# Performance work log

Measured on AMD Instinct MI355X. Metric: run time of the kernel, lower is better.

The kernel has to match this reference:

```python
import jax, jax.numpy as jnp
import numpy as np
from jax.scipy.special import logsumexp

S, D, K, R, P = 500, 768, 16, 256, 64  # seq_len, bert_dim, out_dim, n_pairs, max wordpieces/entity


def setup_inputs() -> dict:
    key = jax.random.key(0)
    k1, k2, k3, k4, k5, k6 = jax.random.split(key, 6)
    word_embeddings = jax.random.normal(k1, (S, D), jnp.float32)
    # kaiming_normal_ fan_in = D*K (last two dims collapsed); gain sqrt(2) for relu
    W = jax.random.normal(k2, (D, K, D), jnp.float32) * np.float32((2.0 / (K * D)) ** 0.5)
    idx1 = jax.random.randint(k3, (R, P), 0, S)
    idx2 = jax.random.randint(k4, (R, P), 0, S)
    # ragged mention lengths -> padding masks (at least 1 valid wordpiece)
    len1 = jax.random.randint(k5, (R,), 1, P + 1)
    len2 = jax.random.randint(k6, (R,), 1, P + 1)
    pos = jnp.arange(P)
    mask1 = (pos[None, :] < len1[:, None]).astype(jnp.float32)
    mask2 = (pos[None, :] < len2[:, None]).astype(jnp.float32)
    return {"word_embeddings": word_embeddings, "W": W, "idx1": idx1, "idx2": idx2,
            "mask1": mask1, "mask2": mask2}


def reference(word_embeddings, W, idx1, idx2, mask1, mask2):
    # gather ragged mention wordpieces (padded to P per entity)
    e1 = word_embeddings[idx1]  # [R, P, D]
    e2 = word_embeddings[idx2]  # [R, P, D]
    # biaffine: z[r,k,p,q] = e1[r,p,:] @ W[:,k,:] @ e2[r,q,:]
    zh = jnp.einsum('rpd,dke->rpke', e1, W)      # [R, P, K, D]
    z = jnp.einsum('rpke,rqe->rkpq', zh, e2)     # [R, K, P, P]
    # logsumexp pooling over all valid (p, q) mention-token pairs
    b = mask1[:, None, :, None] * mask2[:, None, None, :]  # [R, 1, P, P]
    scores = logsumexp(z, axis=(2, 3), b=b)      # [R, K]
    return scores
```

## Files before the change

### kernel.cpp

```cpp
#include <hip/hip_runtime.h>
#include <math.h>

#define S_ 500
#define D_ 768
#define K_ 16
#define R_ 256
#define P_ 64
#define NT 12

typedef unsigned short ushort_t;
typedef __attribute__((ext_vector_type(8))) short short8;
typedef __attribute__((ext_vector_type(4))) float floatx4;

__device__ inline ushort_t f2bf(float x) {
  unsigned int u = __float_as_uint(x);
  u += 0x7fffu + ((u >> 16) & 1u);
  return (ushort_t)(u >> 16);
}

#define GLD_LDS16(g, l)                                                        \
  __builtin_amdgcn_global_load_lds(                                            \
      (const __attribute__((address_space(1))) void*)(g),                      \
      (__attribute__((address_space(3))) void*)(l), 16, 0, 0)

#define ASM_BARRIER asm volatile("s_barrier" ::: "memory")
#define WAIT_VM8 asm volatile("s_waitcnt vmcnt(8)" ::: "memory")
#define WAIT_VM6 asm volatile("s_waitcnt vmcnt(6)" ::: "memory")
#define WAIT_VM0 asm volatile("s_waitcnt vmcnt(0)" ::: "memory")

__global__ __launch_bounds__(256) void prep(const float* __restrict__ WE,
                                            const float* __restrict__ W,
                                            ushort_t* __restrict__ WEb,
                                            ushort_t* __restrict__ Wt) {
  const int t = threadIdx.x;
  if (blockIdx.x < 384) {
    int gid = blockIdx.x * 256 + t;
    int row = gid / 192;
    ushort4 o = {0, 0, 0, 0};
    if (row < S_) {
      float4 v = *(const float4*)(WE + (size_t)gid * 4);
      o.x = f2bf(v.x); o.y = f2bf(v.y); o.z = f2bf(v.z); o.w = f2bf(v.w);
    }
    *(ushort4*)(WEb + (size_t)gid * 4) = o;
    return;
  }
  __shared__ float tile[64][68];
  const int tb = blockIdx.x - 384;
  const int n0 = (tb % 192) * 64, d0 = (tb / 192) * 64;
  {
    const int r = t >> 2, cbase = (t & 3) * 16;
#pragma unroll
    for (int i = 0; i < 4; i++) {
      float4 v = *(const float4*)(W + (size_t)(d0 + r) * 12288 + n0 + cbase + i * 4);
      *(float4*)&tile[r][cbase + i * 4] = v;
    }
  }
  __syncthreads();
  {
    const int bc = t & 15;
    const int br4 = (t >> 4) * 4;
    float4 tv[4];
#pragma unroll
    for (int ii = 0; ii < 4; ii++)
      tv[ii] = *(const float4*)&tile[bc * 4 + ii][br4];
#pragma unroll
    for (int j = 0; j < 4; j++) {
      ushort4 o;
      o.x = f2bf(((const float*)&tv[0])[j]);
      o.y = f2bf(((const float*)&tv[1])[j]);
      o.z = f2bf(((const float*)&tv[2])[j]);
      o.w = f2bf(((const float*)&tv[3])[j]);
      *(ushort4*)(Wt + (size_t)(n0 + br4 + j) * 768 + d0 + bc * 4) = o;
    }
  }
}

__global__ __launch_bounds__(256, 2) void mm0_bt(const ushort_t* __restrict__ A,
                                                 const ushort_t* __restrict__ Bm,
                                                 ushort_t* __restrict__ C) {
  __shared__ ushort_t As[2][2][128 * 32];
  __shared__ ushort_t Bs[2][2][128 * 32];
  const int tid = threadIdx.x;
  const int wave = tid >> 6, lane = tid & 63;
  const int m0 = blockIdx.y * 128, n0 = blockIdx.x * 128;
  const int wm = (wave & 1) * 64, wn = (wave >> 1) * 64;
  const int col = lane & 15, quad = lane >> 4;

  floatx4 acc[4][4];
#pragma unroll
  for (int i = 0; i < 4; i++)
#pragma unroll
    for (int j = 0; j < 4; j++)
#pragma unroll
      for (int e = 0; e < 4; e++) acc[i][j][e] = 0.f;

  const int srow = wave * 32 + (lane >> 2);
  const int scol = (lane & 3) * 8;
  const ushort_t* ga0 = A + (size_t)(m0 + srow) * D_ + scol;
  const ushort_t* gb0 = Bm + (size_t)(n0 + srow) * D_ + scol;
  const int ldsbase = (wave * 32) * 32;

#define ISSUE_TILE0(t_, buf_)                                                  \
  do {                                                                         \
    const ushort_t* ga = ga0 + (t_)*64;                                        \
    const ushort_t* gb = gb0 + (t_)*64;                                        \
    GLD_LDS16(ga, &As[buf_][0][ldsbase]);                                      \
    GLD_LDS16(ga + 16 * D_, &As[buf_][0][ldsbase + 16 * 32]);                  \
    GLD_LDS16(ga + 32, &As[buf_][1][ldsbase]);                                 \
    GLD_LDS16(ga + 32 + 16 * D_, &As[buf_][1][ldsbase + 16 * 32]);             \
    GLD_LDS16(gb, &Bs[buf_][0][ldsbase]);                                      \
    GLD_LDS16(gb + 16 * D_, &Bs[buf_][0][ldsbase + 16 * 32]);                  \
    GLD_LDS16(gb + 32, &Bs[buf_][1][ldsbase]);                                 \
    GLD_LDS16(gb + 32 + 16 * D_, &Bs[buf_][1][ldsbase + 16 * 32]);             \
  } while (0)

  ISSUE_TILE0(0, 0);
  for (int t = 0; t < NT; ++t) {
    const int cur = t & 1;
    if (t + 1 < NT) {
      ISSUE_TILE0(t + 1, cur ^ 1);
      WAIT_VM8;
    } else {
      WAIT_VM0;
    }
    ASM_BARRIER;
#pragma unroll
    for (int s = 0; s < 2; ++s) {
      short8 a[4], b[4];
#pragma unroll
      for (int i = 0; i < 4; i++)
        a[i] = *(const short8*)&As[cur][s][(wm + i * 16 + col) * 32 + quad * 8];
#pragma unroll
      for (int j = 0; j < 4; j++)
        b[j] = *(const short8*)&Bs[cur][s][(wn + j * 16 + col) * 32 + quad * 8];
#pragma unroll
      for (int i = 0; i < 4; i++)
#pragma unroll
        for (int j = 0; j < 4; j++)
          acc[i][j] = __builtin_amdgcn_mfma_f32_16x16x32_bf16(b[j], a[i], acc[i][j], 0, 0, 0);
    }
    ASM_BARRIER;
  }
#undef ISSUE_TILE0

#pragma unroll
  for (int i = 0; i < 4; i++) {
    int m = m0 + wm + i * 16 + col;
#pragma unroll
    for (int j = 0; j < 4; j++) {
      int n = n0 + wn + j * 16 + quad * 4;
      ushort4 o;
      o.x = f2bf(acc[i][j][0]); o.y = f2bf(acc[i][j][1]);
      o.z = f2bf(acc[i][j][2]); o.w = f2bf(acc[i][j][3]);
      *(ushort4*)(C + (size_t)m * 12288 + n) = o;
    }
  }
}

__global__ __launch_bounds__(256, 2) void mm1_bt(const ushort_t* __restrict__ A,
                                                 const ushort_t* __restrict__ Bm,
                                                 ushort_t* __restrict__ G) {
  __shared__ ushort_t As[2][2][128 * 32];
  __shared__ ushort_t Bs[2][2][64 * 32];
  const int tid = threadIdx.x;
  const int wave = tid >> 6, lane = tid & 63;
  const int lin = blockIdx.x + (blockIdx.y << 3);
  const int yb = ((lin & 7) << 3) | (lin >> 6);
  const int xb = (lin >> 3) & 7;
  const int m0 = yb * 128, n0 = xb * 64;
  const int wm = (wave & 1) * 64, wn = (wave >> 1) * 32;
  const int col = lane & 15, quad = lane >> 4;

  floatx4 acc[4][2];
#pragma unroll
  for (int i = 0; i < 4; i++)
#pragma unroll
    for (int j = 0; j < 2; j++)
#pragma unroll
      for (int e = 0; e < 4; e++) acc[i][j][e] = 0.f;

  const int lrow = lane >> 2, scol = (lane & 3) * 8;
  const ushort_t* ga0 = A + (size_t)(m0 + wave * 32 + lrow) * D_ + scol;
  const ushort_t* gb0 = Bm + (size_t)(n0 + wave * 16 + lrow) * D_ + scol;
  const int aoff = (wave * 32) * 32;
  const int boff = (wave * 16) * 32;

#define ISSUE_TILE1(t_, buf_)                                                  \
  do {                                                                         \
    _Pragma("unroll") for (int s_ = 0; s_ < 2; s_++) {                         \
      const ushort_t* ga = ga0 + (t_)*64 + s_ * 32;                            \
      const ushort_t* gb = gb0 + (t_)*64 + s_ * 32;                            \
      GLD_LDS16(ga, &As[buf_][s_][aoff]);                                      \
      GLD_LDS16(ga + 16 * D_, &As[buf_][s_][aoff + 16 * 32]);                  \
      GLD_LDS16(gb, &Bs[buf_][s_][boff]);                                      \
    }                                                                          \
  } while (0)

  ISSUE_TILE1(0, 0);
  for (int t = 0; t < NT; ++t) {
    const int cur = t & 1;
    if (t + 1 < NT) {
      ISSUE_TILE1(t + 1, cur ^ 1);
      WAIT_VM6;
    } else {
      WAIT_VM0;
    }
    ASM_BARRIER;
#pragma unroll
    for (int s = 0; s < 2; ++s) {
      short8 a[4], b[2];
#pragma unroll
      for (int i = 0; i < 4; i++)
        a[i] = *(const short8*)&As[cur][s][(wm + i * 16 + col) * 32 + quad * 8];
#pragma unroll
      for (int j = 0; j < 2; j++)
        b[j] = *(const short8*)&Bs[cur][s][(wn + j * 16 + col) * 32 + quad * 8];
#pragma unroll
      for (int i = 0; i < 4; i++)
#pragma unroll
        for (int j = 0; j < 2; j++)
          acc[i][j] = __builtin_amdgcn_mfma_f32_16x16x32_bf16(a[i], b[j], acc[i][j], 0, 0, 0);
    }
    ASM_BARRIER;
  }
#undef ISSUE_TILE1

#pragma unroll
  for (int i = 0; i < 4; i++) {
    int s1 = (m0 + wm + i * 16) >> 4;
#pragma unroll
    for (int j = 0; j < 2; j++) {
      int s2 = n0 + wn + j * 16 + col;
      if (s1 < S_ && s2 < S_) {
        ushort4 o;
        o.x = f2bf(acc[i][j][0]); o.y = f2bf(acc[i][j][1]);
        o.z = f2bf(acc[i][j][2]); o.w = f2bf(acc[i][j][3]);
        *(ushort4*)(G + (((size_t)s1 * S_ + s2) << 4) + quad * 4) = o;
      }
    }
  }
}

__global__ __launch_bounds__(512) void lse_kernel(const ushort_t* __restrict__ G,
                                                  const int* __restrict__ idx1,
                                                  const int* __restrict__ idx2,
                                                  const float* __restrict__ mask1,
                                                  const float* __restrict__ mask2,
                                                  float* __restrict__ out) {
  const int r = blockIdx.x;
  const int tid = threadIdx.x;
  __shared__ int b1[P_], b2[P_];
  __shared__ int s_len1, s_len2;
  __shared__ float wmx[8][K_], wsum[8][K_];

  if (tid < 64) {
    float mv = mask1[r * P_ + tid];
    unsigned long long bal = __ballot(mv > 0.5f);
    if (tid == 0) s_len1 = (int)__popcll(bal);
    b1[tid] = idx1[r * P_ + tid] * (S_ * K_);
  } else if (tid < 128) {
    int q = tid - 64;
    float mv = mask2[r * P_ + q];
    unsigned long long bal = __ballot(mv > 0.5f);
    if (q == 0) s_len2 = (int)__popcll(bal);
    b2[q] = idx2[r * P_ + q] * K_;
  }
  __syncthreads();
  const int len2 = s_len2;
  const int total = s_len1 * len2;

  float m[K_], s[K_];
#pragma unroll
  for (int k = 0; k < K_; k++) { m[k] = -3.0e38f; s[k] = 0.f; }

  for (int i = tid; i < total; i += 512) {
    int p = i / len2;
    int q = i - p * len2;
    const uint4* g4 = (const uint4*)(G + b1[p] + b2[q]);
    uint4 w0 = g4[0], w1 = g4[1];
    unsigned int uu[8] = {w0.x, w0.y, w0.z, w0.w, w1.x, w1.y, w1.z, w1.w};
    float z[K_];
#pragma unroll
    for (int h = 0; h < 8; h++) {
      z[2 * h + 0] = __uint_as_float(uu[h] << 16);
      z[2 * h + 1] = __uint_as_float(uu[h] & 0xffff0000u);
    }
#pragma unroll
    for (int k = 0; k < K_; k++) {
      float d = z[k] - m[k];
      float e = __expf(-fabsf(d));
      bool up = d > 0.f;
      s[k] = up ? __fmaf_rn(s[k], e, 1.f) : (s[k] + e);
      m[k] = up ? z[k] : m[k];
    }
  }

#pragma unroll
  for (int off = 1; off < 64; off <<= 1) {
#pragma unroll
    for (int k = 0; k < K_; k++) {
      float mo = __shfl_xor(m[k], off, 64);
      float so = __shfl_xor(s[k], off, 64);
      float d = mo - m[k];
      float e = __expf(-fabsf(d));
      bool up = d > 0.f;
      s[k] = up ? __fmaf_rn(s[k], e, so) : __fmaf_rn(so, e, s[k]);
      m[k] = up ? mo : m[k];
    }
  }
  const int wave = tid >> 6, lane = tid & 63;
  if (lane == 0) {
#pragma unroll
    for (int k = 0; k < K_; k++) { wmx[wave][k] = m[k]; wsum[wave][k] = s[k]; }
  }
  __syncthreads();
  if (tid < K_) {
    float M = -3.0e38f, Ssum = 0.f;
#pragma unroll
    for (int w = 0; w < 8; w++) {
      float mo = wmx[w][tid], so = wsum[w][tid];
      float d = mo - M;
      float e = __expf(-fabsf(d));
      bool up = d > 0.f;
      Ssum = up ? __fmaf_rn(Ssum, e, so) : __fmaf_rn(so, e, Ssum);
      M = up ? mo : M;
    }
    out[r * K_ + tid] = M + __logf(Ssum);
  }
}

extern "C" void kernel_launch(void* const* d_in, const int* in_sizes, int n_in,
                              void* d_out, int out_size, void* d_ws, size_t ws_size,
                              hipStream_t stream) {
  const float* WE    = (const float*)d_in[0];
  const float* W     = (const float*)d_in[1];
  const int*   idx1  = (const int*)d_in[2];
  const int*   idx2  = (const int*)d_in[3];
  const float* mask1 = (const float*)d_in[4];
  const float* mask2 = (const float*)d_in[5];
  float* out = (float*)d_out;

  ushort_t* WEb   = (ushort_t*)d_ws;
  ushort_t* Wt    = WEb + (size_t)512 * 768;
  ushort_t* projb = Wt + (size_t)12288 * 768;
  ushort_t* G     = projb + (size_t)8192 * 768;

  prep<<<384 + 2304, 256, 0, stream>>>(WE, W, WEb, Wt);
  mm0_bt<<<dim3(96, 4), 256, 0, stream>>>(WEb, Wt, projb);
  mm1_bt<<<dim3(8, 64), 256, 0, stream>>>(projb, WEb, G);
  lse_kernel<<<R_, 512, 0, stream>>>(G, idx1, idx2, mask1, mask2, out);
}
```

Measured before the change: 134.0 us.

## Fuse W transpose and bf16 conversion into first GEMM's B-tile loads

Drops the separate prep pass that transposed W into a bf16 Wt buffer. The first GEMM now reads fp32 W directly into registers, converts pairs with v_cvt_pk_bf16_f32, and writes them into an XOR-swizzled LDS layout, prefetching the next tile's registers while computing the current one. This removes a full read and write of the 37MB W tensor through a temporary, at the cost of register-staged B loads, a __syncthreads per k-step, and fp32-width global reads inside the GEMM.

```diff
diff --git a/kernel.cpp b/kernel.cpp
--- a/kernel.cpp
+++ b/kernel.cpp
@@ -11,6 +11,7 @@
 typedef unsigned short ushort_t;
 typedef __attribute__((ext_vector_type(8))) short short8;
 typedef __attribute__((ext_vector_type(4))) float floatx4;
+typedef __attribute__((ext_vector_type(4))) float fx4;
 
 __device__ inline ushort_t f2bf(float x) {
   unsigned int u = __float_as_uint(x);
@@ -18,66 +19,37 @@
   return (ushort_t)(u >> 16);
 }
 
+__device__ inline unsigned int cvtpk(float lo, float hi) {
+  unsigned int r;
+  asm("v_cvt_pk_bf16_f32 %0, %1, %2" : "=v"(r) : "v"(lo), "v"(hi));
+  return r;
+}
+
 #define GLD_LDS16(g, l)                                                        \
   __builtin_amdgcn_global_load_lds(                                            \
       (const __attribute__((address_space(1))) void*)(g),                      \
       (__attribute__((address_space(3))) void*)(l), 16, 0, 0)
 
 #define ASM_BARRIER asm volatile("s_barrier" ::: "memory")
-#define WAIT_VM8 asm volatile("s_waitcnt vmcnt(8)" ::: "memory")
 #define WAIT_VM6 asm volatile("s_waitcnt vmcnt(6)" ::: "memory")
 #define WAIT_VM0 asm volatile("s_waitcnt vmcnt(0)" ::: "memory")
 
 __global__ __launch_bounds__(256) void prep(const float* __restrict__ WE,
-                                            const float* __restrict__ W,
-                                            ushort_t* __restrict__ WEb,
-                                            ushort_t* __restrict__ Wt) {
+                                            ushort_t* __restrict__ WEb) {
   const int t = threadIdx.x;
-  if (blockIdx.x < 384) {
-    int gid = blockIdx.x * 256 + t;
-    int row = gid / 192;
-    ushort4 o = {0, 0, 0, 0};
-    if (row < S_) {
-      float4 v = *(const float4*)(WE + (size_t)gid * 4);
-      o.x = f2bf(v.x); o.y = f2bf(v.y); o.z = f2bf(v.z); o.w = f2bf(v.w);
-    }
-    *(ushort4*)(WEb + (size_t)gid * 4) = o;
-    return;
-  }
-  __shared__ float tile[64][68];
-  const int tb = blockIdx.x - 384;
-  const int n0 = (tb % 192) * 64, d0 = (tb / 192) * 64;
-  {
-    const int r = t >> 2, cbase = (t & 3) * 16;
-#pragma unroll
-    for (int i = 0; i < 4; i++) {
-      float4 v = *(const float4*)(W + (size_t)(d0 + r) * 12288 + n0 + cbase + i * 4);
-      *(float4*)&tile[r][cbase + i * 4] = v;
-    }
-  }
-  __syncthreads();
-  {
-    const int bc = t & 15;
-    const int br4 = (t >> 4) * 4;
-    float4 tv[4];
-#pragma unroll
-    for (int ii = 0; ii < 4; ii++)
-      tv[ii] = *(const float4*)&tile[bc * 4 + ii][br4];
-#pragma unroll
-    for (int j = 0; j < 4; j++) {
-      ushort4 o;
-      o.x = f2bf(((const float*)&tv[0])[j]);
-      o.y = f2bf(((const float*)&tv[1])[j]);
-      o.z = f2bf(((const float*)&tv[2])[j]);
-      o.w = f2bf(((const float*)&tv[3])[j]);
-      *(ushort4*)(Wt + (size_t)(n0 + br4 + j) * 768 + d0 + bc * 4) = o;
-    }
-  }
-}
-
-__global__ __launch_bounds__(256, 2) void mm0_bt(const ushort_t* __restrict__ A,
-                                                 const ushort_t* __restrict__ Bm,
-                                                 ushort_t* __restrict__ C) {
+  int gid = blockIdx.x * 256 + t;
+  int row = gid / 192;
+  ushort4 o = {0, 0, 0, 0};
+  if (row < S_) {
+    float4 v = *(const float4*)(WE + (size_t)gid * 4);
+    o.x = f2bf(v.x); o.y = f2bf(v.y); o.z = f2bf(v.z); o.w = f2bf(v.w);
+  }
+  *(ushort4*)(WEb + (size_t)gid * 4) = o;
+}
+
+__global__ __launch_bounds__(256, 2) void mm0_fused(const ushort_t* __restrict__ A,
+                                                    const float* __restrict__ Wf,
+                                                    ushort_t* __restrict__ C) {
   __shared__ ushort_t As[2][2][128 * 32];
   __shared__ ushort_t Bs[2][2][128 * 32];
   const int tid = threadIdx.x;
@@ -97,33 +69,54 @@
   const int srow = wave * 32 + (lane >> 2);
   const int scol = (lane & 3) * 8;
   const ushort_t* ga0 = A + (size_t)(m0 + srow) * D_ + scol;
-  const ushort_t* gb0 = Bm + (size_t)(n0 + srow) * D_ + scol;
   const int ldsbase = (wave * 32) * 32;
 
-#define ISSUE_TILE0(t_, buf_)                                                  \
+#define ISSUE_A(t_, buf_)                                                      \
   do {                                                                         \
     const ushort_t* ga = ga0 + (t_)*64;                                        \
-    const ushort_t* gb = gb0 + (t_)*64;                                        \
     GLD_LDS16(ga, &As[buf_][0][ldsbase]);                                      \
     GLD_LDS16(ga + 16 * D_, &As[buf_][0][ldsbase + 16 * 32]);                  \
     GLD_LDS16(ga + 32, &As[buf_][1][ldsbase]);                                 \
     GLD_LDS16(ga + 32 + 16 * D_, &As[buf_][1][ldsbase + 16 * 32]);             \
-    GLD_LDS16(gb, &Bs[buf_][0][ldsbase]);                                      \
-    GLD_LDS16(gb + 16 * D_, &Bs[buf_][0][ldsbase + 16 * 32]);                  \
-    GLD_LDS16(gb + 32, &Bs[buf_][1][ldsbase]);                                 \
-    GLD_LDS16(gb + 32 + 16 * D_, &Bs[buf_][1][ldsbase + 16 * 32]);             \
   } while (0)
 
-  ISSUE_TILE0(0, 0);
+  const int nq = tid & 31;
+  const int dqA = tid >> 5;
+  const float* gwA = Wf + (size_t)(dqA * 4) * 12288 + n0 + nq * 4;
+  const float* gwB = gwA + (size_t)32 * 12288;
+
+  fx4 bv[2][4];
+#define LOADB(t_)                                                              \
+  do {                                                                         \
+    _Pragma("unroll") for (int i = 0; i < 4; i++) {                            \
+      bv[0][i] = *(const fx4*)(gwA + (size_t)((t_)*64 + i) * 12288);           \
+      bv[1][i] = *(const fx4*)(gwB + (size_t)((t_)*64 + i) * 12288);           \
+    }                                                                          \
+  } while (0)
+
+#define WRITEB(buf_)                                                           \
+  do {                                                                         \
+    _Pragma("unroll") for (int h = 0; h < 2; h++)                              \
+    _Pragma("unroll") for (int j = 0; j < 4; j++) {                            \
+      int row = nq * 4 + j;                                                    \
+      uint2 w;                                                                 \
+      w.x = cvtpk(bv[h][0][j], bv[h][1][j]);                                   \
+      w.y = cvtpk(bv[h][2][j], bv[h][3][j]);                                   \
+      *(uint2*)((char*)&Bs[buf_][h][0] +                                       \
+                ((row * 64 + dqA * 8) ^ ((nq & 15) << 4))) = w;                \
+    }                                                                          \
+  } while (0)
+
+  ISSUE_A(0, 0);
+  LOADB(0);
   for (int t = 0; t < NT; ++t) {
     const int cur = t & 1;
+    WRITEB(cur);
+    __syncthreads();
     if (t + 1 < NT) {
-      ISSUE_TILE0(t + 1, cur ^ 1);
-      WAIT_VM8;
-    } else {
-      WAIT_VM0;
-    }
-    ASM_BARRIER;
+      ISSUE_A(t + 1, cur ^ 1);
+      LOADB(t + 1);
+    }
 #pragma unroll
     for (int s = 0; s < 2; ++s) {
       short8 a[4], b[4];
@@ -131,17 +124,21 @@
       for (int i = 0; i < 4; i++)
         a[i] = *(const short8*)&As[cur][s][(wm + i * 16 + col) * 32 + quad * 8];
 #pragma unroll
-      for (int j = 0; j < 4; j++)
-        b[j] = *(const short8*)&Bs[cur][s][(wn + j * 16 + col) * 32 + quad * 8];
+      for (int j = 0; j < 4; j++) {
+        int row = wn + j * 16 + col;
+        b[j] = *(const short8*)((const char*)&Bs[cur][s][0] +
+                                ((row * 64 + quad * 16) ^ (((row >> 2) & 15) << 4)));
+      }
 #pragma unroll
       for (int i = 0; i < 4; i++)
 #pragma unroll
         for (int j = 0; j < 4; j++)
           acc[i][j] = __builtin_amdgcn_mfma_f32_16x16x32_bf16(b[j], a[i], acc[i][j], 0, 0, 0);
     }
-    ASM_BARRIER;
-  }
-#undef ISSUE_TILE0
+  }
+#undef ISSUE_A
+#undef LOADB
+#undef WRITEB
 
 #pragma unroll
   for (int i = 0; i < 4; i++) {
@@ -341,12 +338,11 @@
   float* out = (float*)d_out;
 
   ushort_t* WEb   = (ushort_t*)d_ws;
-  ushort_t* Wt    = WEb + (size_t)512 * 768;
-  ushort_t* projb = Wt + (size_t)12288 * 768;
-  ushort_t* G     = projb + (size_t)8192 * 768;
-
-  prep<<<384 + 2304, 256, 0, stream>>>(WE, W, WEb, Wt);
-  mm0_bt<<<dim3(96, 4), 256, 0, stream>>>(WEb, Wt, projb);
+  ushort_t* projb = WEb + (size_t)512 * 768;
+  ushort_t* G     = projb + (size_t)512 * 12288;
+
+  prep<<<384, 256, 0, stream>>>(WE, WEb);
+  mm0_fused<<<dim3(96, 4), 256, 0, stream>>>(WEb, W, projb);
   mm1_bt<<<dim3(8, 64), 256, 0, stream>>>(projb, WEb, G);
   lse_kernel<<<R_, 512, 0, stream>>>(G, idx1, idx2, mask1, mask2, out);
 }
```

Measured after the change: 133.8 us. About the same (-0.2%).
